# Kernel tuning notes

Hardware: AMD Instinct MI355X
Metric: run time of the kernel (lower is better)

Reference implementation:

```python
import jax, jax.numpy as jnp
import numpy as np

G, N, F_IN, D, R, E, L = 512, 128, 64, 128, 4, 1572864, 2  # graphs, nodes/graph, in-feat, embed, relations, edges, gnn layers


def setup_inputs() -> dict:
    key = jax.random.key(0)
    ks = jax.random.split(key, 8)
    x = jax.random.normal(ks[0], (G * N, F_IN), jnp.float32)
    # edges are within-graph (disjoint batched graph, as built by batch_to_gd)
    gid = jax.random.randint(ks[1], (E,), 0, G)
    loc = jax.random.randint(ks[2], (2, E), 0, N)
    edge_index = gid[None, :] * N + loc  # [2, E] (src, dst)
    edge_attr = jax.random.randint(ks[3], (E,), 0, R)
    W_emb = jax.random.normal(ks[4], (F_IN, D), jnp.float32) / np.sqrt(F_IN)
    b_emb = jnp.zeros((D,), jnp.float32)
    W_root = jax.random.normal(ks[5], (L, D, D), jnp.float32) / np.sqrt(D)
    W_rel = jax.random.normal(ks[6], (L, R, D, D), jnp.float32) / np.sqrt(D)
    bias = jnp.zeros((L, D), jnp.float32)
    return {"x": x, "edge_index": edge_index, "edge_attr": edge_attr,
            "W_emb": W_emb, "b_emb": b_emb, "W_root": W_root, "W_rel": W_rel, "bias": bias}


def rgcn_layer(h, edge_index, edge_attr, W_root_l, W_rel_l, bias_l):
    # PyG RGCNConv: out_i = h_i @ W_root + sum_r mean_{j in N_r(i)} (h_j @ W_r) + bias
    n = h.shape[0]
    xr = jnp.einsum('nd,rde->rne', h, W_rel_l)          # [R, n, D] per-relation transform
    src, dst = edge_index[0], edge_index[1]
    msg = xr[edge_attr, src]                             # [E, D] gather per edge
    seg = dst * R + edge_attr                            # combined (node, relation) segment id
    summed = jax.ops.segment_sum(msg, seg, num_segments=n * R)
    cnt = jax.ops.segment_sum(jnp.ones((msg.shape[0],), h.dtype), seg, num_segments=n * R)
    mean = summed / jnp.maximum(cnt, 1.0)[:, None]       # per-relation mean aggregation
    agg = mean.reshape(n, R, -1).sum(axis=1)             # sum over relations
    return h @ W_root_l + agg + bias_l


def reference(x, edge_index, edge_attr, W_emb, b_emb, W_root, W_rel, bias):
    h = x @ W_emb + b_emb                                # embedding_linear
    for l in range(L):                                   # mp_rounds = 1 per layer
        h = jax.nn.relu(rgcn_layer(h, edge_index, edge_attr, W_root[l], W_rel[l], bias[l]))
    # split into per-graph chunks of N nodes and max-pool over nodes
    return jnp.max(h.reshape(G, N, -1), axis=1)          # [G, D]
```

## Files before the change

### kernel.cpp

```cpp
#include <hip/hip_runtime.h>

constexpr int GG    = 512;
constexpr int NPG   = 128;
constexpr int FIN   = 64;
constexpr int DD    = 128;
constexpr int RR    = 4;
constexpr int NN    = GG * NPG;
constexpr int EE    = 1572864;
constexpr int SLC   = 4096;
constexpr int HSTR  = 136;

typedef __attribute__((ext_vector_type(8))) short bf16x8;
typedef __attribute__((ext_vector_type(4))) float f32x4;
typedef __attribute__((ext_vector_type(2))) float f32x2;
typedef unsigned short u16;
typedef unsigned int   u32;

__device__ __forceinline__ u32 bf16_rne(float x) {
    u32 u = __float_as_uint(x);
    return (u + 0x7FFFu + ((u >> 16) & 1u)) >> 16;
}

__device__ __forceinline__ void gl_lds16(const void* g, void* l) {
    __builtin_amdgcn_global_load_lds((const __attribute__((address_space(1))) u32*)g,
                                     (__attribute__((address_space(3))) u32*)l, 16, 0, 0);
}


__global__ __launch_bounds__(256, 2) void k_front(const int* __restrict__ ei,
                                                  const int* __restrict__ ea,
                                                  u32* __restrict__ bcur,
                                                  u16* __restrict__ binned,
                                                  const float* __restrict__ W_root,
                                                  const float* __restrict__ W_rel,
                                                  const float* __restrict__ W_emb,
                                                  u16* __restrict__ wtH) {
    __shared__ u32 sRec[4096];
    __shared__ int bh[512];
    __shared__ int lcur[512];
    __shared__ float tile[32 * 129];
    int tid = threadIdx.x;
    int bid = blockIdx.x;

    if (bid < 384) {
        int e0 = bid * 4096;
        bh[tid] = 0; bh[tid + 256] = 0;
        __syncthreads();
        for (int i = 0; i < 16; ++i) {
            int e = e0 + i * 256 + tid;
            int src = ei[e];
            int dst = ei[EE + e];
            int a   = ea[e];
            int g   = dst >> 7;
            u32 rec = (u32)(src & 127) | ((u32)(dst & 127) << 7) | ((u32)a << 14);
            sRec[i * 256 + tid] = rec | ((u32)g << 16);
            atomicAdd(&bh[g], 1);
        }
        __syncthreads();
        lcur[tid]       = tid * SLC +
                          (int)atomicAdd(&bcur[tid], (u32)bh[tid]);
        lcur[tid + 256] = (tid + 256) * SLC +
                          (int)atomicAdd(&bcur[tid + 256], (u32)bh[tid + 256]);
        __syncthreads();
        for (int i = 0; i < 16; ++i) {
            u32 r = sRec[i * 256 + tid];
            int pos = atomicAdd(&lcur[r >> 16], 1);
            binned[pos] = (u16)(r & 0xFFFFu);
        }
    } else if (bid < 424) {
        int pb = bid - 384;
        int mat = pb >> 2;
        int k0 = (pb & 3) * 32;
        int l = mat / 5, m5 = mat - l * 5;
        const float* Wsrc = (m5 == 0) ? (W_root + l * 16384)
                                      : (W_rel + (size_t)(l * RR + (m5 - 1)) * 16384);
        for (int i = 0; i < 16; ++i) {
            int k = k0 + (tid >> 7) + i * 2;
            int n = tid & 127;
            tile[(k - k0) * 129 + n] = Wsrc[k * 128 + n];
        }
        __syncthreads();
        for (int i = 0; i < 16; ++i) {
            int kk = tid & 31;
            int n  = (tid >> 5) + i * 8;
            wtH[mat * 16384 + n * 128 + k0 + kk] = (u16)bf16_rne(tile[kk * 129 + n]);
        }
    } else {
        int k0 = (bid - 424) * 32;
        for (int i = 0; i < 16; ++i) {
            int k = k0 + (tid >> 7) + i * 2;
            int n = tid & 127;
            tile[(k - k0) * 129 + n] = W_emb[k * 128 + n];
        }
        __syncthreads();
        for (int i = 0; i < 16; ++i) {
            int kk = tid & 31;
            int n  = (tid >> 5) + i * 8;
            wtH[163840 + n * 64 + k0 + kk] = (u16)bf16_rne(tile[kk * 129 + n]);
        }
    }
}


__global__ __launch_bounds__(512, 4) void k_fused(const float* __restrict__ x,
                                                  const float* __restrict__ b_emb,
                                                  float* __restrict__ outF,
                                                  const u16* __restrict__ wtH,
                                                  const float* __restrict__ bias,
                                                  const u16* __restrict__ binned,
                                                  const u32* __restrict__ bcur) {
    __shared__ __align__(16) u16 hG[128 * HSTR];
    __shared__ __align__(16) u16 sQ[2][8192];
    __shared__ __align__(16) u16 sIdx[SLC];
    __shared__ int   sOffs[512];
    __shared__ int   sCnt[512];
    __shared__ float sInv[512];

    int tid  = threadIdx.x;
    int wave = tid >> 6, lane = tid & 63;
    int mm   = lane & 15;
    int qd   = lane >> 4;
    int gr   = blockIdx.x;
    int row0g = gr * NPG;
    int strip = wave * 16;
    const u16* wtE = wtH + 163840;

    auto stage = [&](int step, int bufi) {
        const u16* src = wtH + (step >> 1) * 16384 + (step & 1) * 64;
#pragma unroll
        for (int i = 0; i < 2; ++i) {
            int u = i * 512 + tid;
            int n = u >> 3, j = u & 7;
            gl_lds16(src + n * 128 + ((j ^ (n & 7)) * 8), &sQ[bufi][u * 8]);
        }
    };
    auto stageE = [&](int bufi) {
#pragma unroll
        for (int i = 0; i < 2; ++i) {
            int u = i * 512 + tid;
            int n = u >> 3, j = u & 7;
            gl_lds16(wtE + n * 64 + ((j ^ (n & 7)) * 8), &sQ[bufi][u * 8]);
        }
    };

    f32x4 acc[8];
    auto mfma_half = [&](int bufi, bf16x8 A0, bf16x8 A1) {
        const u16* buf = sQ[bufi];
#pragma unroll
        for (int nt = 0; nt < 8; ++nt) {
            int n = nt * 16 + mm;
            int g0 = n * 8 + ((0 * 4 + qd) ^ (n & 7));
            int g1 = n * 8 + ((1 * 4 + qd) ^ (n & 7));
            bf16x8 B0 = *(const bf16x8*)&buf[g0 * 8];
            bf16x8 B1 = *(const bf16x8*)&buf[g1 * 8];
            f32x4 a = acc[nt];
            a = __builtin_amdgcn_mfma_f32_16x16x32_bf16(A0, B0, a, 0, 0, 0);
            a = __builtin_amdgcn_mfma_f32_16x16x32_bf16(A1, B1, a, 0, 0, 0);
            acc[nt] = a;
        }
    };

    auto gather = [&](int rel, bf16x8* AH) {
        int key = (rel << 7) + strip + mm;
        int r0 = sOffs[key];
        int r1 = sCnt[key];
        float s = sInv[key];
#pragma unroll
        for (int h = 0; h < 2; ++h) {
            int cb = h * 64 + qd * 8;
            f32x2 ax[8];
#pragma unroll
            for (int i = 0; i < 8; ++i) ax[i] = (f32x2){0.f, 0.f};
            auto upk8 = [&](int ks, uint4 u) {
                ax[ks*4+0] += (f32x2){__uint_as_float(u.x << 16),
                                      __uint_as_float(u.x & 0xffff0000u)};
                ax[ks*4+1] += (f32x2){__uint_as_float(u.y << 16),
                                      __uint_as_float(u.y & 0xffff0000u)};
                ax[ks*4+2] += (f32x2){__uint_as_float(u.z << 16),
                                      __uint_as_float(u.z & 0xffff0000u)};
                ax[ks*4+3] += (f32x2){__uint_as_float(u.w << 16),
                                      __uint_as_float(u.w & 0xffff0000u)};
            };
            int j = r0;
            for (; j + 2 <= r1; j += 2) {
                int rb0 = (int)sIdx[j]     * HSTR + cb;
                int rb1 = (int)sIdx[j + 1] * HSTR + cb;
                uint4 a0 = *(const uint4*)&hG[rb0];
                uint4 a1 = *(const uint4*)&hG[rb0 + 32];
                uint4 b0 = *(const uint4*)&hG[rb1];
                uint4 b1 = *(const uint4*)&hG[rb1 + 32];
                upk8(0, a0); upk8(1, a1); upk8(0, b0); upk8(1, b1);
            }
            if (j < r1) {
                int rb = (int)sIdx[j] * HSTR + cb;
                uint4 a0 = *(const uint4*)&hG[rb];
                uint4 a1 = *(const uint4*)&hG[rb + 32];
                upk8(0, a0); upk8(1, a1);
            }
#pragma unroll
            for (int k2 = 0; k2 < 2; ++k2) {
                uint4 u;
                u.x = bf16_rne(ax[k2*4+0].x * s) | (bf16_rne(ax[k2*4+0].y * s) << 16);
                u.y = bf16_rne(ax[k2*4+1].x * s) | (bf16_rne(ax[k2*4+1].y * s) << 16);
                u.z = bf16_rne(ax[k2*4+2].x * s) | (bf16_rne(ax[k2*4+2].y * s) << 16);
                u.w = bf16_rne(ax[k2*4+3].x * s) | (bf16_rne(ax[k2*4+3].y * s) << 16);
                AH[h * 2 + k2] = *(bf16x8*)&u;
            }
        }
    };

    stageE(0);
    int cnt = (int)bcur[gr];
    if (cnt > SLC) cnt = SLC;
    uint4 myRec = *(const uint4*)&binned[gr * SLC + tid * 8];
    sCnt[tid] = 0;
    __syncthreads();
    int base8 = tid * 8;
#pragma unroll
    for (int i = 0; i < 8; ++i) {
        if (base8 + i < cnt) {
            u32 w = ((const u32*)&myRec)[i >> 1];
            u32 rec = (i & 1) ? (w >> 16) : (w & 0xFFFFu);
            atomicAdd(&sCnt[rec >> 7], 1);
        }
    }
    __syncthreads();
    int c = sCnt[tid];
    int v = c;
#pragma unroll
    for (int o = 1; o < 64; o <<= 1) {
        int t = __shfl_up(v, o);
        if (lane >= o) v += t;
    }
    int* wtot = (int*)sIdx;
    if (lane == 63) wtot[wave] = v;
    __syncthreads();
    int base = 0;
#pragma unroll
    for (int w = 0; w < 8; ++w) {
        int tw = wtot[w];
        if (w < wave) base += tw;
    }
    int ex = base + v - c;
    sOffs[tid] = ex;
    sCnt[tid]  = ex;
    sInv[tid]  = 1.0f / (float)(c > 0 ? c : 1);
    __syncthreads();
#pragma unroll
    for (int i = 0; i < 8; ++i) {
        if (base8 + i < cnt) {
            u32 w = ((const u32*)&myRec)[i >> 1];
            u32 rec = (i & 1) ? (w >> 16) : (w & 0xFFFFu);
            int pos = atomicAdd(&sCnt[rec >> 7], 1);
            sIdx[pos] = (u16)(rec & 127u);
        }
    }
    __syncthreads();

    {
#pragma unroll
        for (int nt = 0; nt < 8; ++nt) {
            float bv = b_emb[nt * 16 + mm];
            acc[nt] = (f32x4){bv, bv, bv, bv};
        }
        bf16x8 AE[2];
#pragma unroll
        for (int ks = 0; ks < 2; ++ks) {
            const float* xp = &x[(size_t)(row0g + strip + mm) * FIN + ks * 32 + qd * 8];
            float4 a = *(const float4*)xp;
            float4 b = *(const float4*)(xp + 4);
            uint4 u;
            u.x = bf16_rne(a.x) | (bf16_rne(a.y) << 16);
            u.y = bf16_rne(a.z) | (bf16_rne(a.w) << 16);
            u.z = bf16_rne(b.x) | (bf16_rne(b.y) << 16);
            u.w = bf16_rne(b.z) | (bf16_rne(b.w) << 16);
            AE[ks] = *(bf16x8*)&u;
        }
        stage(0, 1);
        mfma_half(0, AE[0], AE[1]);
#pragma unroll
        for (int nt = 0; nt < 8; ++nt)
#pragma unroll
            for (int r = 0; r < 4; ++r)
                hG[(strip + qd * 4 + r) * HSTR + nt * 16 + mm] =
                    (u16)bf16_rne(acc[nt][r]);
        __syncthreads();
    }

    for (int L = 0; L < 2; ++L) {
        const float* bl = bias + L * DD;
#pragma unroll
        for (int i = 0; i < 8; ++i) acc[i] = (f32x4){0.f, 0.f, 0.f, 0.f};

        bf16x8 AH[4];
#pragma unroll
        for (int ks = 0; ks < 4; ++ks)
            AH[ks] = *(const bf16x8*)&hG[(strip + mm) * HSTR + ks * 32 + qd * 8];

        for (int m = 0; m < 5; ++m) {
#pragma unroll
            for (int h = 0; h < 2; ++h) {
                int s = L * 10 + m * 2 + h;
                if (s + 1 < 20) stage(s + 1, s & 1);
                mfma_half((s + 1) & 1, AH[h * 2], AH[h * 2 + 1]);
                __syncthreads();
            }
            if (m < 4) gather(m, AH);
        }

        if (L == 0) {
#pragma unroll
            for (int nt = 0; nt < 8; ++nt) {
                float bv = bl[nt * 16 + mm];
#pragma unroll
                for (int r = 0; r < 4; ++r)
                    hG[(strip + qd * 4 + r) * HSTR + nt * 16 + mm] =
                        (u16)bf16_rne(fmaxf(acc[nt][r] + bv, 0.f));
            }
            __syncthreads();
        } else {
            float* red = (float*)sIdx;
#pragma unroll
            for (int nt = 0; nt < 8; ++nt) {
                float bv = bl[nt * 16 + mm];
                float vv = fmaxf(fmaxf(acc[nt][0], acc[nt][1]),
                                 fmaxf(acc[nt][2], acc[nt][3])) + bv;
                vv = fmaxf(vv, 0.f);
                vv = fmaxf(vv, __shfl_xor(vv, 16));
                vv = fmaxf(vv, __shfl_xor(vv, 32));
                if (lane < 16) red[wave * 128 + nt * 16 + mm] = vv;
            }
            __syncthreads();
            if (tid < 128) {
                float mx = red[tid];
#pragma unroll
                for (int w = 1; w < 8; ++w) mx = fmaxf(mx, red[w * 128 + tid]);
                outF[gr * DD + tid] = mx;
            }
        }
    }
}


extern "C" void kernel_launch(void* const* d_in, const int* in_sizes, int n_in,
                              void* d_out, int out_size, void* d_ws, size_t ws_size,
                              hipStream_t stream) {
    const float* x      = (const float*)d_in[0];
    const int*   ei     = (const int*)  d_in[1];
    const int*   ea     = (const int*)  d_in[2];
    const float* W_emb  = (const float*)d_in[3];
    const float* b_emb  = (const float*)d_in[4];
    const float* W_root = (const float*)d_in[5];
    const float* W_rel  = (const float*)d_in[6];
    const float* bias   = (const float*)d_in[7];
    float* out = (float*)d_out;

    char* p = (char*)d_ws;
    u32* bcur   = (u32*)p; p += 2048;
    u16* binned = (u16*)p; p += (size_t)GG * SLC * 2;
    u16* wtH    = (u16*)p; p += (size_t)(10 * 16384 + 8192) * 2;

    (void)hipMemsetAsync(bcur, 0, 2048, stream);

    k_front<<<426, 256, 0, stream>>>(ei, ea, bcur, binned,
                                     W_root, W_rel, W_emb, wtH);
    k_fused<<<GG, 512, 0, stream>>>(x, b_emb, out, wtH, bias, binned, bcur);
}
```

Measured before the change: 184.3 us.

## Read weight B-fragments directly from global memory instead of LDS double-buffer staging

Removes the LDS double-buffered weight staging (global_load_lds into sQ) and the per-half-step block barriers, and instead has each wave load its MFMA B operands straight from global/L2 memory. This cuts the 32 KB of LDS per block, which may allow more resident blocks, and removes many __syncthreads. The trade-off is that every wave now re-reads the same weight tiles from cache with no prefetch overlap, so MFMAs may stall on global-load latency. Barriers are added before the hG writeback so the gather reads stay safe.

Result: slower. 265.4 us (+44.0%).

```diff
diff --git a/kernel.cpp b/kernel.cpp
--- a/kernel.cpp
+++ b/kernel.cpp
@@ -19,11 +19,6 @@
 __device__ __forceinline__ u32 bf16_rne(float x) {
     u32 u = __float_as_uint(x);
     return (u + 0x7FFFu + ((u >> 16) & 1u)) >> 16;
-}
-
-__device__ __forceinline__ void gl_lds16(const void* g, void* l) {
-    __builtin_amdgcn_global_load_lds((const __attribute__((address_space(1))) u32*)g,
-                                     (__attribute__((address_space(3))) u32*)l, 16, 0, 0);
 }
 
 
@@ -110,7 +105,6 @@
                                                   const u16* __restrict__ binned,
                                                   const u32* __restrict__ bcur) {
     __shared__ __align__(16) u16 hG[128 * HSTR];
-    __shared__ __align__(16) u16 sQ[2][8192];
     __shared__ __align__(16) u16 sIdx[SLC];
     __shared__ int   sOffs[512];
     __shared__ int   sCnt[512];
@@ -125,37 +119,21 @@
     int strip = wave * 16;
     const u16* wtE = wtH + 163840;
 
-    auto stage = [&](int step, int bufi) {
-        const u16* src = wtH + (step >> 1) * 16384 + (step & 1) * 64;
-#pragma unroll
-        for (int i = 0; i < 2; ++i) {
-            int u = i * 512 + tid;
-            int n = u >> 3, j = u & 7;
-            gl_lds16(src + n * 128 + ((j ^ (n & 7)) * 8), &sQ[bufi][u * 8]);
-        }
-    };
-    auto stageE = [&](int bufi) {
-#pragma unroll
-        for (int i = 0; i < 2; ++i) {
-            int u = i * 512 + tid;
-            int n = u >> 3, j = u & 7;
-            gl_lds16(wtE + n * 64 + ((j ^ (n & 7)) * 8), &sQ[bufi][u * 8]);
-        }
-    };
-
     f32x4 acc[8];
-    auto mfma_half = [&](int bufi, bf16x8 A0, bf16x8 A1) {
-        const u16* buf = sQ[bufi];
+
+    auto do_mat = [&](const u16* __restrict__ W, const bf16x8* AH) {
 #pragma unroll
         for (int nt = 0; nt < 8; ++nt) {
-            int n = nt * 16 + mm;
-            int g0 = n * 8 + ((0 * 4 + qd) ^ (n & 7));
-            int g1 = n * 8 + ((1 * 4 + qd) ^ (n & 7));
-            bf16x8 B0 = *(const bf16x8*)&buf[g0 * 8];
-            bf16x8 B1 = *(const bf16x8*)&buf[g1 * 8];
+            const u16* bp = W + (nt * 16 + mm) * 128 + qd * 8;
+            bf16x8 B0 = *(const bf16x8*)(bp);
+            bf16x8 B1 = *(const bf16x8*)(bp + 32);
+            bf16x8 B2 = *(const bf16x8*)(bp + 64);
+            bf16x8 B3 = *(const bf16x8*)(bp + 96);
             f32x4 a = acc[nt];
-            a = __builtin_amdgcn_mfma_f32_16x16x32_bf16(A0, B0, a, 0, 0, 0);
-            a = __builtin_amdgcn_mfma_f32_16x16x32_bf16(A1, B1, a, 0, 0, 0);
+            a = __builtin_amdgcn_mfma_f32_16x16x32_bf16(AH[0], B0, a, 0, 0, 0);
+            a = __builtin_amdgcn_mfma_f32_16x16x32_bf16(AH[1], B1, a, 0, 0, 0);
+            a = __builtin_amdgcn_mfma_f32_16x16x32_bf16(AH[2], B2, a, 0, 0, 0);
+            a = __builtin_amdgcn_mfma_f32_16x16x32_bf16(AH[3], B3, a, 0, 0, 0);
             acc[nt] = a;
         }
     };
@@ -209,7 +187,6 @@
         }
     };
 
-    stageE(0);
     int cnt = (int)bcur[gr];
     if (cnt > SLC) cnt = SLC;
     uint4 myRec = *(const uint4*)&binned[gr * SLC + tid * 8];
@@ -276,8 +253,16 @@
             u.w = bf16_rne(b.z) | (bf16_rne(b.w) << 16);
             AE[ks] = *(bf16x8*)&u;
         }
-        stage(0, 1);
-        mfma_half(0, AE[0], AE[1]);
+#pragma unroll
+        for (int nt = 0; nt < 8; ++nt) {
+            const u16* bp = wtE + (nt * 16 + mm) * 64 + qd * 8;
+            bf16x8 B0 = *(const bf16x8*)(bp);
+            bf16x8 B1 = *(const bf16x8*)(bp + 32);
+            f32x4 a = acc[nt];
+            a = __builtin_amdgcn_mfma_f32_16x16x32_bf16(AE[0], B0, a, 0, 0, 0);
+            a = __builtin_amdgcn_mfma_f32_16x16x32_bf16(AE[1], B1, a, 0, 0, 0);
+            acc[nt] = a;
+        }
 #pragma unroll
         for (int nt = 0; nt < 8; ++nt)
 #pragma unroll
@@ -298,17 +283,12 @@
             AH[ks] = *(const bf16x8*)&hG[(strip + mm) * HSTR + ks * 32 + qd * 8];
 
         for (int m = 0; m < 5; ++m) {
-#pragma unroll
-            for (int h = 0; h < 2; ++h) {
-                int s = L * 10 + m * 2 + h;
-                if (s + 1 < 20) stage(s + 1, s & 1);
-                mfma_half((s + 1) & 1, AH[h * 2], AH[h * 2 + 1]);
-                __syncthreads();
-            }
+            do_mat(wtH + (L * 5 + m) * 16384, AH);
             if (m < 4) gather(m, AH);
         }
 
         if (L == 0) {
+            __syncthreads();
 #pragma unroll
             for (int nt = 0; nt < 8; ++nt) {
                 float bv = bl[nt * 16 + mm];
@@ -319,6 +299,7 @@
             }
             __syncthreads();
         } else {
+            __syncthreads();
             float* red = (float*)sIdx;
 #pragma unroll
             for (int nt = 0; nt < 8; ++nt) {
```
